# Kernel optimization log

Hardware: AMD Instinct MI355X
Metric: run time of the kernel (lower is better)

## Reference

```python
import jax, jax.numpy as jnp
import numpy as np

EPS = 1e-5
NUM_HEADS = 8
BLOCK_SIZE = 8


def _ln(x, w, b):
    mu = jnp.mean(x, axis=-1, keepdims=True)
    var = jnp.mean((x - mu) ** 2, axis=-1, keepdims=True)
    return (x - mu) * jax.lax.rsqrt(var + EPS) * w + b


def _mha(x, wqkv, bqkv, wo, bo, allowed):
    # x: [b,t,d]; wqkv: [3d,d]; allowed: [t,t] bool (True = attend)
    b, t, d = x.shape
    h, hd = NUM_HEADS, d // NUM_HEADS
    qkv = x @ wqkv.T + bqkv
    q, k, v = jnp.split(qkv, 3, axis=-1)
    q = q.reshape(b, t, h, hd)
    k = k.reshape(b, t, h, hd)
    v = v.reshape(b, t, h, hd)
    scores = jnp.einsum('bihd,bjhd->bhij', q, k) / np.sqrt(hd).astype(x.dtype)
    scores = jnp.where(allowed[None, None], scores, -jnp.inf)
    attn = jax.nn.softmax(scores, axis=-1)
    out = jnp.einsum('bhij,bjhd->bihd', attn, v).reshape(b, t, d)
    return out @ wo.T + bo


def setup_inputs() -> dict:
    key = jax.random.key(0)
    ks = jax.random.split(key, 20)
    B, T, D, FF, L, MAXT = 64, 512, 256, 512, 4, 512
    s = 0.02
    return {
        'latents': jax.random.normal(ks[0], (B, T, D), dtype=jnp.float32),
        'move_ids': jax.random.randint(ks[1], (B, T), 0, 20480),
        'mask': jax.random.randint(ks[2], (B, T), 0, 2).astype(bool),
        'positional': s * jax.random.normal(ks[3], (1, MAXT, D), dtype=jnp.float32),
        'embed_from': s * jax.random.normal(ks[4], (64, D), dtype=jnp.float32),
        'embed_to': s * jax.random.normal(ks[5], (64, D), dtype=jnp.float32),
        'embed_promo': s * jax.random.normal(ks[6], (5, D), dtype=jnp.float32),
        'in_proj_w': s * jax.random.normal(ks[7], (L, 3 * D, D), dtype=jnp.float32),
        'in_proj_b': jnp.zeros((L, 3 * D), dtype=jnp.float32),
        'out_w': s * jax.random.normal(ks[8], (L, D, D), dtype=jnp.float32),
        'out_b': jnp.zeros((L, D), dtype=jnp.float32),
        'fc1_w': s * jax.random.normal(ks[9], (L, FF, D), dtype=jnp.float32),
        'fc1_b': jnp.zeros((L, FF), dtype=jnp.float32),
        'fc2_w': s * jax.random.normal(ks[10], (L, D, FF), dtype=jnp.float32),
        'fc2_b': jnp.zeros((L, D), dtype=jnp.float32),
        'norm_w': jnp.ones((D,), dtype=jnp.float32),
        'norm_b': jnp.zeros((D,), dtype=jnp.float32),
    }


def reference(latents, move_ids, mask, positional, embed_from, embed_to,
              embed_promo, in_proj_w, in_proj_b, out_w, out_b,
              fc1_w, fc1_b, fc2_w, fc2_b, norm_w, norm_b):
    b, t, d = latents.shape
    # move-id decomposition: promo/from/to embedding sum
    promo = move_ids // 4096
    rem = move_ids % 4096
    frm = rem // 64
    to = rem % 64
    x = latents + positional[:, :t, :] + embed_from[frm] + embed_to[to] + embed_promo[promo]
    # block-causal mask: token i may attend j iff block(j) <= block(i)
    bidx = jnp.arange(t) // BLOCK_SIZE
    allowed = bidx[None, :] <= bidx[:, None]
    n_layers = in_proj_w.shape[0]
    for l in range(n_layers):
        # NOTE: the single LayerNorm (norm_w, norm_b) is shared everywhere,
        # exactly as in the original module.
        x = x + _mha(_ln(x, norm_w, norm_b), in_proj_w[l], in_proj_b[l],
                     out_w[l], out_b[l], allowed)
        h1 = jax.nn.relu(_ln(x, norm_w, norm_b) @ fc1_w[l].T + fc1_b[l])
        x = x + h1 @ fc2_w[l].T + fc2_b[l]
    x = _ln(x, norm_w, norm_b)
    return jnp.where(mask[..., None], x, latents)
```

## Files before the change

kernel.cpp:

```cpp
#include <hip/hip_runtime.h>
#include <math.h>

#define Bv  64
#define Tv  512
#define Dv  256
#define FFv 512
#define Lv  4
#define BTv (Bv*Tv)
#define EPSv 1e-5f
#define RS32 0.17677669529663687f

typedef __attribute__((ext_vector_type(8))) short short8;
typedef __attribute__((ext_vector_type(4))) float f32x4;
typedef unsigned short us;

__device__ __forceinline__ us f2bf(float f) {
    union { float f; unsigned u; } v; v.f = f;
    unsigned u = v.u + 0x7FFFu + ((v.u >> 16) & 1u);
    return (us)(u >> 16);
}
__device__ __forceinline__ unsigned pk2(float a, float b) {
    return ((unsigned)f2bf(b) << 16) | (unsigned)f2bf(a);
}
__device__ __forceinline__ float wave_sum(float v) {
#pragma unroll
    for (int o = 32; o > 0; o >>= 1) v += __shfl_xor(v, o);
    return v;
}

__global__ __launch_bounds__(256) void cvtall_kernel(
    const float* __restrict__ qw, const float* __restrict__ ow,
    const float* __restrict__ f1, const float* __restrict__ f2,
    const float* __restrict__ qb,
    us* __restrict__ wq, us* __restrict__ wo, us* __restrict__ w1,
    us* __restrict__ w2, float* __restrict__ sb)
{
    int blk = blockIdx.x, tid = threadIdx.x;
    if (blk < 2048) {
        const float* s; us* d; int i; float sc = 1.0f;
        if (blk < 768)       { i = blk*256 + tid;        s = qw; d = wq;
                               sc = (((i >> 6) % 768) < 256) ? RS32 : 1.0f; }
        else if (blk < 1024) { i = (blk-768)*256 + tid;  s = ow; d = wo; }
        else if (blk < 1536) { i = (blk-1024)*256 + tid; s = f1; d = w1; }
        else                 { i = (blk-1536)*256 + tid; s = f2; d = w2; }
        float4 v = ((const float4*)s)[i];
        ushort4 o;
        o.x = f2bf(v.x*sc); o.y = f2bf(v.y*sc); o.z = f2bf(v.z*sc); o.w = f2bf(v.w*sc);
        ((ushort4*)d)[i] = o;
    } else {
        int i = (blk-2048)*256 + tid;
        sb[i] = qb[i] * (((i % 768) < 256) ? RS32 : 1.0f);
    }
}

__global__ __launch_bounds__(256) void embed_ln_kernel(
    const float* __restrict__ lat, const int* __restrict__ mids,
    const float* __restrict__ pos, const float* __restrict__ ef,
    const float* __restrict__ et,  const float* __restrict__ ep,
    const float* __restrict__ nw,  const float* __restrict__ nb,
    float* __restrict__ x, us* __restrict__ xn)
{
    int bt = blockIdx.x;
    int d  = threadIdx.x;
    int t  = bt & (Tv - 1);
    int id = mids[bt];
    int promo = id >> 12;
    int rem   = id & 4095;
    int frm   = rem >> 6;
    int to    = rem & 63;
    size_t o = (size_t)bt * Dv + d;
    float xv = lat[o] + pos[t*Dv + d] + ef[frm*Dv + d] + et[to*Dv + d] + ep[promo*Dv + d];
    x[o] = xv;
    __shared__ float rs[4], rq[4];
    int wv = d >> 6, lane = d & 63;
    float s  = wave_sum(xv);
    float sq = wave_sum(xv*xv);
    if (lane == 0) { rs[wv] = s; rq[wv] = sq; }
    __syncthreads();
    float mu  = (rs[0]+rs[1]+rs[2]+rs[3]) * (1.0f/Dv);
    float var = (rq[0]+rq[1]+rq[2]+rq[3]) * (1.0f/Dv) - mu*mu;
    float inv = rsqrtf(var + EPSv);
    xn[o] = f2bf((xv - mu)*inv*nw[d] + nb[d]);
}

__global__ __launch_bounds__(256) void final_kernel(
    const float* __restrict__ x, const float* __restrict__ lat,
    const int* __restrict__ mask, const float* __restrict__ w,
    const float* __restrict__ b, float* __restrict__ out)
{
    int wv = threadIdx.x >> 6, lane = threadIdx.x & 63;
    size_t row = (size_t)blockIdx.x * 4 + wv;
    float4 v = ((const float4*)(x + row*Dv))[lane];
    float mu = wave_sum(v.x + v.y + v.z + v.w) * (1.0f/Dv);
    float dx = v.x-mu, dy = v.y-mu, dz = v.z-mu, dw = v.w-mu;
    float var = wave_sum(dx*dx + dy*dy + dz*dz + dw*dw) * (1.0f/Dv);
    float inv = rsqrtf(var + EPSv);
    float4 w4 = ((const float4*)w)[lane];
    float4 b4 = ((const float4*)b)[lane];
    float4 o;
    o.x = dx*inv*w4.x + b4.x;
    o.y = dy*inv*w4.y + b4.y;
    o.z = dz*inv*w4.z + b4.z;
    o.w = dw*inv*w4.w + b4.w;
    if (!mask[row]) o = ((const float4*)(lat + row*Dv))[lane];
    ((float4*)(out + row*Dv))[lane] = o;
}

template<int RELU>
__global__ __launch_bounds__(256) void mm_kernel(
    const us* __restrict__ A, const us* __restrict__ B,
    const float* __restrict__ bias, us* __restrict__ C,
    int M, int N, int K)
{
    __shared__ us As[128*64];
    __shared__ us Bs[128*64];
    int tid  = threadIdx.x;
    int lane = tid & 63;
    int wu   = __builtin_amdgcn_readfirstlane(tid >> 6);
    int m0 = blockIdx.x * 128, n0 = blockIdx.y * 128;
    int wm = wu & 1, wn = wu >> 1;
    f32x4 acc[4][4] = {};
    int srow = lane >> 3;
    int sg   = (lane & 7) ^ srow;
    const us* Ag = A + (size_t)m0 * K + sg*8;
    const us* Bg = B + (size_t)n0 * K + sg*8;
    int cc = lane & 15, q4 = lane >> 4;
    for (int k0 = 0; k0 < K; k0 += 64) {
        __syncthreads();
#pragma unroll
        for (int p = 0; p < 4; p++) {
            int row = wu*32 + p*8;
            __builtin_amdgcn_global_load_lds(
                (const __attribute__((address_space(1))) unsigned int*)(Ag + (size_t)(row + srow)*K + k0),
                (__attribute__((address_space(3))) unsigned int*)(As + row*64),
                16, 0, 0);
            __builtin_amdgcn_global_load_lds(
                (const __attribute__((address_space(1))) unsigned int*)(Bg + (size_t)(row + srow)*K + k0),
                (__attribute__((address_space(3))) unsigned int*)(Bs + row*64),
                16, 0, 0);
        }
        __syncthreads();
#pragma unroll
        for (int h = 0; h < 2; h++) {
            int pg = ((h*4 + q4) ^ (cc & 7)) * 8;
            short8 av[4], bv[4];
#pragma unroll
            for (int i = 0; i < 4; i++)
                av[i] = *(const short8*)(As + (wm*64 + i*16 + cc)*64 + pg);
#pragma unroll
            for (int j = 0; j < 4; j++)
                bv[j] = *(const short8*)(Bs + (wn*64 + j*16 + cc)*64 + pg);
#pragma unroll
            for (int i = 0; i < 4; i++)
#pragma unroll
                for (int j = 0; j < 4; j++)
                    acc[i][j] = __builtin_amdgcn_mfma_f32_16x16x32_bf16(av[i], bv[j], acc[i][j], 0, 0, 0);
        }
    }
#pragma unroll
    for (int j = 0; j < 4; j++) {
        int n = n0 + wn*64 + j*16 + cc;
        float bj = bias[n];
#pragma unroll
        for (int i = 0; i < 4; i++) {
#pragma unroll
            for (int r = 0; r < 4; r++) {
                int m = m0 + wm*64 + i*16 + q4*4 + r;
                float v = acc[i][j][r] + bj;
                if (RELU) v = fmaxf(v, 0.f);
                C[(size_t)m * N + n] = f2bf(v);
            }
        }
    }
}

__global__ __launch_bounds__(256) void mm256_kernel(
    const us* __restrict__ A, const us* __restrict__ B,
    const float* __restrict__ bias, float* __restrict__ x,
    us* __restrict__ xn, const float* __restrict__ nw,
    const float* __restrict__ nb, int M, int K)
{
    __shared__ us As[64*64];
    __shared__ us Bs[256*64];
    __shared__ float red[64][4][2];
    __shared__ float mus[64], rss[64];
    int tid  = threadIdx.x;
    int lane = tid & 63;
    int wu   = __builtin_amdgcn_readfirstlane(tid >> 6);
    int m0 = blockIdx.x * 64;
    f32x4 acc[4][4] = {};
    int srow = lane >> 3;
    int sg   = (lane & 7) ^ srow;
    const us* Ag = A + (size_t)m0 * K + sg*8;
    const us* Bg = B + sg*8;
    int cc = lane & 15, q4 = lane >> 4;
    for (int k0 = 0; k0 < K; k0 += 64) {
        __syncthreads();
#pragma unroll
        for (int p = 0; p < 2; p++) {
            int row = wu*16 + p*8;
            __builtin_amdgcn_global_load_lds(
                (const __attribute__((address_space(1))) unsigned int*)(Ag + (size_t)(row + srow)*K + k0),
                (__attribute__((address_space(3))) unsigned int*)(As + row*64),
                16, 0, 0);
        }
#pragma unroll
        for (int p = 0; p < 8; p++) {
            int row = wu*64 + p*8;
            __builtin_amdgcn_global_load_lds(
                (const __attribute__((address_space(1))) unsigned int*)(Bg + (size_t)(row + srow)*K + k0),
                (__attribute__((address_space(3))) unsigned int*)(Bs + row*64),
                16, 0, 0);
        }
        __syncthreads();
#pragma unroll
        for (int h = 0; h < 2; h++) {
            int pg = ((h*4 + q4) ^ (cc & 7)) * 8;
            short8 av[4], bv[4];
#pragma unroll
            for (int i = 0; i < 4; i++)
                av[i] = *(const short8*)(As + (i*16 + cc)*64 + pg);
#pragma unroll
            for (int j = 0; j < 4; j++)
                bv[j] = *(const short8*)(Bs + (wu*64 + j*16 + cc)*64 + pg);
#pragma unroll
            for (int i = 0; i < 4; i++)
#pragma unroll
                for (int j = 0; j < 4; j++)
                    acc[i][j] = __builtin_amdgcn_mfma_f32_16x16x32_bf16(av[i], bv[j], acc[i][j], 0, 0, 0);
        }
    }
    float bb[4], nwv[4], nbv[4];
#pragma unroll
    for (int j = 0; j < 4; j++) {
        int n = wu*64 + j*16 + cc;
        bb[j] = bias[n]; nwv[j] = nw[n]; nbv[j] = nb[n];
    }
#pragma unroll
    for (int i = 0; i < 4; i++) {
        float s[4] = {0.f,0.f,0.f,0.f}, sq[4] = {0.f,0.f,0.f,0.f};
#pragma unroll
        for (int j = 0; j < 4; j++) {
#pragma unroll
            for (int r = 0; r < 4; r++) {
                int m = m0 + i*16 + q4*4 + r;
                size_t off = (size_t)m * Dv + wu*64 + j*16 + cc;
                float v = acc[i][j][r] + bb[j] + x[off];
                acc[i][j][r] = v;
                x[off] = v;
                s[r] += v; sq[r] += v*v;
            }
        }
#pragma unroll
        for (int r = 0; r < 4; r++) {
#pragma unroll
            for (int o = 1; o < 16; o <<= 1) {
                s[r]  += __shfl_xor(s[r],  o);
                sq[r] += __shfl_xor(sq[r], o);
            }
        }
        if (cc == 0) {
#pragma unroll
            for (int r = 0; r < 4; r++) {
                red[i*16 + q4*4 + r][wu][0] = s[r];
                red[i*16 + q4*4 + r][wu][1] = sq[r];
            }
        }
    }
    __syncthreads();
    if (tid < 64) {
        float ts = red[tid][0][0] + red[tid][1][0] + red[tid][2][0] + red[tid][3][0];
        float tq = red[tid][0][1] + red[tid][1][1] + red[tid][2][1] + red[tid][3][1];
        float mu = ts * (1.0f/Dv);
        float var = tq * (1.0f/Dv) - mu*mu;
        mus[tid] = mu;
        rss[tid] = rsqrtf(var + EPSv);
    }
    __syncthreads();
#pragma unroll
    for (int i = 0; i < 4; i++) {
#pragma unroll
        for (int r = 0; r < 4; r++) {
            int ml = i*16 + q4*4 + r;
            float mu = mus[ml], rv = rss[ml];
#pragma unroll
            for (int j = 0; j < 4; j++) {
                size_t off = (size_t)(m0 + ml) * Dv + wu*64 + j*16 + cc;
                xn[off] = f2bf((acc[i][j][r] - mu)*rv*nwv[j] + nbv[j]);
            }
        }
    }
}

__global__ __launch_bounds__(512) void ffn_kernel(
    const us* __restrict__ W1, const float* __restrict__ b1,
    const us* __restrict__ W2, const float* __restrict__ b2,
    float* __restrict__ x, us* xn,
    const float* __restrict__ nw, const float* __restrict__ nb)
{
    __shared__ us Axn[4*64*64];
    __shared__ us bufB[64*520];
    __shared__ float red[64][2][2];
    __shared__ float mus[64], rss[64];

    int tid  = threadIdx.x;
    int lane = tid & 63;
    int wu   = __builtin_amdgcn_readfirstlane(tid >> 6);
    int m0   = blockIdx.x * 64;
    int srow = lane >> 3;
    int sg   = (lane & 7) ^ srow;
    int cc = lane & 15, q4 = lane >> 4;
    int rw  = (wu & 3) * 16;
    int cw  = (wu >> 2) * 256;
    int cw2 = (wu >> 2) * 128;

#pragma unroll
    for (int j4 = 0; j4 < 4; j4++) {
        int j = wu*4 + j4;
        int kt = j >> 3, p = j & 7;
        __builtin_amdgcn_global_load_lds(
            (const __attribute__((address_space(1))) unsigned int*)(xn + (size_t)(m0 + p*8 + srow)*256 + kt*64 + sg*8),
            (__attribute__((address_space(3))) unsigned int*)(Axn + kt*4096 + p*512),
            16, 0, 0);
    }

    f32x4 acc1[16] = {};
    for (int kt = 0; kt < 4; kt++) {
        __syncthreads();
#pragma unroll
        for (int jj = 0; jj < 8; jj++) {
            int j = wu*8 + jj;
            __builtin_amdgcn_global_load_lds(
                (const __attribute__((address_space(1))) unsigned int*)(W1 + (size_t)(j*8 + srow)*256 + kt*64 + sg*8),
                (__attribute__((address_space(3))) unsigned int*)(bufB + j*512),
                16, 0, 0);
        }
        __syncthreads();
#pragma unroll
        for (int h2 = 0; h2 < 2; h2++) {
            int pg = ((h2*4 + q4) ^ (cc & 7)) * 8;
            short8 af = *(const short8*)(Axn + kt*4096 + (rw + cc)*64 + pg);
#pragma unroll
            for (int jj = 0; jj < 16; jj++) {
                short8 bf = *(const short8*)(bufB + (cw + jj*16 + cc)*64 + pg);
                acc1[jj] = __builtin_amdgcn_mfma_f32_16x16x32_bf16(af, bf, acc1[jj], 0, 0, 0);
            }
        }
    }
    __syncthreads();
#pragma unroll
    for (int jj = 0; jj < 16; jj++) {
        int n = cw + jj*16 + cc;
        float bb = b1[n];
#pragma unroll
        for (int r = 0; r < 4; r++) {
            float v = fmaxf(acc1[jj][r] + bb, 0.f);
            bufB[(rw + q4*4 + r)*520 + n] = f2bf(v);
        }
    }

    f32x4 acc2[8] = {};
    for (int kt2 = 0; kt2 < 8; kt2++) {
        __syncthreads();
#pragma unroll
        for (int j4 = 0; j4 < 4; j4++) {
            int j = wu*4 + j4;
            __builtin_amdgcn_global_load_lds(
                (const __attribute__((address_space(1))) unsigned int*)(W2 + (size_t)(j*8 + srow)*512 + kt2*64 + sg*8),
                (__attribute__((address_space(3))) unsigned int*)(Axn + j*512),
                16, 0, 0);
        }
        __syncthreads();
#pragma unroll
        for (int h2 = 0; h2 < 2; h2++) {
            short8 af = *(const short8*)(bufB + (rw + cc)*520 + kt2*64 + (h2*4 + q4)*8);
            int pg = ((h2*4 + q4) ^ (cc & 7)) * 8;
#pragma unroll
            for (int j2 = 0; j2 < 8; j2++) {
                short8 bf = *(const short8*)(Axn + (cw2 + j2*16 + cc)*64 + pg);
                acc2[j2] = __builtin_amdgcn_mfma_f32_16x16x32_bf16(af, bf, acc2[j2], 0, 0, 0);
            }
        }
    }

    float bb2[8], nwv[8], nbv[8];
#pragma unroll
    for (int j2 = 0; j2 < 8; j2++) {
        int n = cw2 + j2*16 + cc;
        bb2[j2] = b2[n]; nwv[j2] = nw[n]; nbv[j2] = nb[n];
    }
    float s[4] = {0.f,0.f,0.f,0.f}, sq[4] = {0.f,0.f,0.f,0.f};
#pragma unroll
    for (int j2 = 0; j2 < 8; j2++) {
#pragma unroll
        for (int r = 0; r < 4; r++) {
            size_t off = (size_t)(m0 + rw + q4*4 + r) * Dv + cw2 + j2*16 + cc;
            float v = acc2[j2][r] + bb2[j2] + x[off];
            acc2[j2][r] = v;
            x[off] = v;
            s[r] += v; sq[r] += v*v;
        }
    }
#pragma unroll
    for (int r = 0; r < 4; r++) {
#pragma unroll
        for (int o = 1; o < 16; o <<= 1) {
            s[r]  += __shfl_xor(s[r],  o);
            sq[r] += __shfl_xor(sq[r], o);
        }
    }
    if (cc == 0) {
#pragma unroll
        for (int r = 0; r < 4; r++) {
            red[rw + q4*4 + r][wu >> 2][0] = s[r];
            red[rw + q4*4 + r][wu >> 2][1] = sq[r];
        }
    }
    __syncthreads();
    if (tid < 64) {
        float ts = red[tid][0][0] + red[tid][1][0];
        float tq = red[tid][0][1] + red[tid][1][1];
        float mu = ts * (1.0f/Dv);
        float var = tq * (1.0f/Dv) - mu*mu;
        mus[tid] = mu;
        rss[tid] = rsqrtf(var + EPSv);
    }
    __syncthreads();
#pragma unroll
    for (int r = 0; r < 4; r++) {
        int ml = rw + q4*4 + r;
        float mu = mus[ml], rv = rss[ml];
#pragma unroll
        for (int j2 = 0; j2 < 8; j2++) {
            size_t off = (size_t)(m0 + ml) * Dv + cw2 + j2*16 + cc;
            xn[off] = f2bf((acc2[j2][r] - mu)*rv*nwv[j2] + nbv[j2]);
        }
    }
}

__global__ __launch_bounds__(256) void attn_kernel(
    const us* __restrict__ qkv, us* __restrict__ ao)
{
    int blk = blockIdx.x;
    int b  = blk & 63;
    int h  = (blk >> 6) & 7;
    int qt = blk >> 9;
    int i0 = qt << 6;
    int tid = threadIdx.x;
    int lane = tid & 63;
    int wu = tid >> 6;

    __shared__ us Ks[2][64][40];
    __shared__ us Vt[2][32][72];
    __shared__ us Ps[4][16][72];
    __shared__ float Ls[4][16];

    size_t rowbase = (size_t)b * Tv;
    int c = lane & 15, q4 = lane >> 4;

    short8 qfrag = *(const short8*)(qkv + (rowbase + i0 + wu*16 + c)*768 + h*32 + q4*8);

    int skey = tid >> 2, sdc = (tid & 3) << 3;
    int vkey = tid & 63, vg = tid >> 6;
    const us* kgp = qkv + (rowbase + skey)*768 + 256 + h*32 + sdc;
    const us* vgp = qkv + (rowbase + vkey)*768 + 512 + h*32 + vg*8;

    f32x4 oacc[2] = {};
    float lsum = 0.f;
    int ntiles = qt + 1;

    short8 kreg = *(const short8*)(kgp);
    short8 vreg = *(const short8*)(vgp);
    *(short8*)&Ks[0][skey][sdc] = kreg;
#pragma unroll
    for (int j = 0; j < 8; j++) Vt[0][vg*8 + j][vkey] = vreg[j];
    if (ntiles > 1) {
        kreg = *(const short8*)(kgp + 64*768);
        vreg = *(const short8*)(vgp + 64*768);
    }
    __syncthreads();

    for (int kt = 0; kt < ntiles; kt++) {
        int cur = kt & 1;
        if (kt + 1 < ntiles) {
            *(short8*)&Ks[cur^1][skey][sdc] = kreg;
#pragma unroll
            for (int j = 0; j < 8; j++) Vt[cur^1][vg*8 + j][vkey] = vreg[j];
        }
        if (kt + 2 < ntiles) {
            kreg = *(const short8*)(kgp + (size_t)(kt+2)*64*768);
            vreg = *(const short8*)(vgp + (size_t)(kt+2)*64*768);
        }

        f32x4 st[4];
#pragma unroll
        for (int jt = 0; jt < 4; jt++) {
            short8 kf = *(const short8*)&Ks[cur][jt*16 + c][q4*8];
            st[jt] = __builtin_amdgcn_mfma_f32_16x16x32_bf16(kf, qfrag, (f32x4){0.f,0.f,0.f,0.f}, 0, 0, 0);
        }
        bool diag = (kt == ntiles - 1);
#pragma unroll
        for (int jt = 0; jt < 4; jt++) {
            float msk = (!diag || (2*jt + (q4 >> 1) <= 2*wu + (c >> 3))) ? 1.f : 0.f;
            float p0 = __expf(st[jt][0]) * msk;
            float p1 = __expf(st[jt][1]) * msk;
            float p2 = __expf(st[jt][2]) * msk;
            float p3 = __expf(st[jt][3]) * msk;
            lsum += p0 + p1 + p2 + p3;
            uint2 w2; w2.x = pk2(p0, p1); w2.y = pk2(p2, p3);
            *(uint2*)&Ps[wu][c][jt*16 + q4*4] = w2;
        }
#pragma unroll
        for (int kk = 0; kk < 2; kk++) {
            short8 pf = *(const short8*)&Ps[wu][c][kk*32 + q4*8];
#pragma unroll
            for (int dt = 0; dt < 2; dt++) {
                short8 vf = *(const short8*)&Vt[cur][dt*16 + c][kk*32 + q4*8];
                oacc[dt] = __builtin_amdgcn_mfma_f32_16x16x32_bf16(pf, vf, oacc[dt], 0, 0, 0);
            }
        }
        __syncthreads();
    }

    float l = lsum;
    l += __shfl_xor(l, 16);
    l += __shfl_xor(l, 32);
    if (q4 == 0) Ls[wu][c] = 1.0f / l;
    float4 lv4 = *(const float4*)&Ls[wu][q4*4];
#pragma unroll
    for (int dt = 0; dt < 2; dt++) {
#pragma unroll
        for (int r = 0; r < 4; r++) {
            float li = (r == 0) ? lv4.x : (r == 1) ? lv4.y : (r == 2) ? lv4.z : lv4.w;
            ao[(rowbase + i0 + wu*16 + q4*4 + r)*256 + h*32 + dt*16 + c] = f2bf(oacc[dt][r] * li);
        }
    }
}

extern "C" void kernel_launch(void* const* d_in, const int* in_sizes, int n_in,
                              void* d_out, int out_size, void* d_ws, size_t ws_size,
                              hipStream_t stream)
{
    const float* latents    = (const float*)d_in[0];
    const int*   move_ids   = (const int*)  d_in[1];
    const int*   mask       = (const int*)  d_in[2];
    const float* positional = (const float*)d_in[3];
    const float* embed_from = (const float*)d_in[4];
    const float* embed_to   = (const float*)d_in[5];
    const float* embed_promo= (const float*)d_in[6];
    const float* in_proj_w  = (const float*)d_in[7];
    const float* in_proj_b  = (const float*)d_in[8];
    const float* out_w      = (const float*)d_in[9];
    const float* out_b      = (const float*)d_in[10];
    const float* fc1_w      = (const float*)d_in[11];
    const float* fc1_b      = (const float*)d_in[12];
    const float* fc2_w      = (const float*)d_in[13];
    const float* fc2_b      = (const float*)d_in[14];
    const float* norm_w     = (const float*)d_in[15];
    const float* norm_b     = (const float*)d_in[16];
    float* out = (float*)d_out;

    float* x   = (float*)d_ws;
    float* sb  = x + (size_t)BTv * Dv;
    us* xn  = (us*)(sb + Lv*768);
    us* qkv = xn + (size_t)BTv * Dv;
    us* ao  = qkv + (size_t)BTv * 768;
    us* h1  = ao + (size_t)BTv * Dv;
    us* wq  = h1 + (size_t)BTv * FFv;
    us* wo  = wq + (size_t)Lv * 768 * Dv;
    us* w1  = wo + (size_t)Lv * Dv * Dv;
    us* w2  = w1 + (size_t)Lv * FFv * Dv;

    cvtall_kernel<<<2060, 256, 0, stream>>>(in_proj_w, out_w, fc1_w, fc2_w,
                                            in_proj_b, wq, wo, w1, w2, sb);

    embed_ln_kernel<<<BTv, 256, 0, stream>>>(latents, move_ids, positional,
        embed_from, embed_to, embed_promo, norm_w, norm_b, x, xn);

    for (int l = 0; l < Lv; l++) {
        mm_kernel<0><<<dim3(BTv/128, 768/128), 256, 0, stream>>>(
            xn, wq + (size_t)l*768*Dv, sb + l*768, qkv, BTv, 768, Dv);
        attn_kernel<<<Bv*8*(Tv/64), 256, 0, stream>>>(qkv, ao);
        mm256_kernel<<<BTv/64, 256, 0, stream>>>(
            ao, wo + (size_t)l*Dv*Dv, out_b + l*Dv, x, xn, norm_w, norm_b,
            BTv, Dv);
        ffn_kernel<<<BTv/64, 512, 0, stream>>>(
            w1 + (size_t)l*FFv*Dv, fc1_b + l*FFv,
            w2 + (size_t)l*Dv*FFv, fc2_b + l*Dv,
            x, xn, norm_w, norm_b);
    }
    final_kernel<<<BTv/4, 256, 0, stream>>>(x, latents, mask, norm_w, norm_b, out);
}
```

Measured before the change: 652.1 us.

## Load FFN weights directly from global into registers instead of staging in LDS

The FFN kernel stops staging activation and weight tiles through LDS with global_load_lds and barriers. Each wave now loads its A fragments and W1/W2 fragments straight from global memory into registers, and keeps only the hidden activation tile in LDS. It also adds a min-blocks-per-CU hint to launch bounds to raise occupancy. This removes most barriers and LDS traffic, but gives up cooperative reuse, so each wave issues many more global loads (partly served from cache) and register pressure rises.

```diff
diff --git a/kernel.cpp b/kernel.cpp
--- a/kernel.cpp
+++ b/kernel.cpp
@@ -292,14 +292,13 @@
     }
 }
 
-__global__ __launch_bounds__(512) void ffn_kernel(
+__global__ __launch_bounds__(512, 4) void ffn_kernel(
     const us* __restrict__ W1, const float* __restrict__ b1,
     const us* __restrict__ W2, const float* __restrict__ b2,
     float* __restrict__ x, us* xn,
     const float* __restrict__ nw, const float* __restrict__ nb)
 {
-    __shared__ us Axn[4*64*64];
-    __shared__ us bufB[64*520];
+    __shared__ us h1s[64*520];
     __shared__ float red[64][2][2];
     __shared__ float mus[64], rss[64];
 
@@ -307,78 +306,54 @@
     int lane = tid & 63;
     int wu   = __builtin_amdgcn_readfirstlane(tid >> 6);
     int m0   = blockIdx.x * 64;
-    int srow = lane >> 3;
-    int sg   = (lane & 7) ^ srow;
     int cc = lane & 15, q4 = lane >> 4;
     int rw  = (wu & 3) * 16;
     int cw  = (wu >> 2) * 256;
     int cw2 = (wu >> 2) * 128;
 
-#pragma unroll
-    for (int j4 = 0; j4 < 4; j4++) {
-        int j = wu*4 + j4;
-        int kt = j >> 3, p = j & 7;
-        __builtin_amdgcn_global_load_lds(
-            (const __attribute__((address_space(1))) unsigned int*)(xn + (size_t)(m0 + p*8 + srow)*256 + kt*64 + sg*8),
-            (__attribute__((address_space(3))) unsigned int*)(Axn + kt*4096 + p*512),
-            16, 0, 0);
-    }
-
-    f32x4 acc1[16] = {};
-    for (int kt = 0; kt < 4; kt++) {
-        __syncthreads();
-#pragma unroll
-        for (int jj = 0; jj < 8; jj++) {
-            int j = wu*8 + jj;
-            __builtin_amdgcn_global_load_lds(
-                (const __attribute__((address_space(1))) unsigned int*)(W1 + (size_t)(j*8 + srow)*256 + kt*64 + sg*8),
-                (__attribute__((address_space(3))) unsigned int*)(bufB + j*512),
-                16, 0, 0);
-        }
-        __syncthreads();
-#pragma unroll
-        for (int h2 = 0; h2 < 2; h2++) {
-            int pg = ((h2*4 + q4) ^ (cc & 7)) * 8;
-            short8 af = *(const short8*)(Axn + kt*4096 + (rw + cc)*64 + pg);
-#pragma unroll
-            for (int jj = 0; jj < 16; jj++) {
-                short8 bf = *(const short8*)(bufB + (cw + jj*16 + cc)*64 + pg);
-                acc1[jj] = __builtin_amdgcn_mfma_f32_16x16x32_bf16(af, bf, acc1[jj], 0, 0, 0);
-            }
-        }
-    }
-    __syncthreads();
-#pragma unroll
-    for (int jj = 0; jj < 16; jj++) {
-        int n = cw + jj*16 + cc;
-        float bb = b1[n];
-#pragma unroll
-        for (int r = 0; r < 4; r++) {
-            float v = fmaxf(acc1[jj][r] + bb, 0.f);
-            bufB[(rw + q4*4 + r)*520 + n] = f2bf(v);
-        }
-    }
+    short8 av[8];
+    {
+        const us* xrow = xn + (size_t)(m0 + rw + cc) * 256 + q4*8;
+#pragma unroll
+        for (int t = 0; t < 8; t++)
+            av[t] = *(const short8*)(xrow + t*32);
+    }
+    {
+        const us* w1p = W1 + (size_t)(cw + cc) * 256 + q4*8;
+#pragma unroll 4
+        for (int jj = 0; jj < 16; jj++) {
+            f32x4 acc = {0.f, 0.f, 0.f, 0.f};
+#pragma unroll
+            for (int t = 0; t < 8; t++) {
+                short8 bf = *(const short8*)(w1p + (size_t)jj*16*256 + t*32);
+                acc = __builtin_amdgcn_mfma_f32_16x16x32_bf16(av[t], bf, acc, 0, 0, 0);
+            }
+            int n = cw + jj*16 + cc;
+            float bb = b1[n];
+#pragma unroll
+            for (int r = 0; r < 4; r++) {
+                float v = fmaxf(acc[r] + bb, 0.f);
+                h1s[(rw + q4*4 + r)*520 + n] = f2bf(v);
+            }
+        }
+    }
+    __syncthreads();
 
     f32x4 acc2[8] = {};
-    for (int kt2 = 0; kt2 < 8; kt2++) {
-        __syncthreads();
-#pragma unroll
-        for (int j4 = 0; j4 < 4; j4++) {
-            int j = wu*4 + j4;
-            __builtin_amdgcn_global_load_lds(
-                (const __attribute__((address_space(1))) unsigned int*)(W2 + (size_t)(j*8 + srow)*512 + kt2*64 + sg*8),
-                (__attribute__((address_space(3))) unsigned int*)(Axn + j*512),
-                16, 0, 0);
-        }
-        __syncthreads();
-#pragma unroll
-        for (int h2 = 0; h2 < 2; h2++) {
-            short8 af = *(const short8*)(bufB + (rw + cc)*520 + kt2*64 + (h2*4 + q4)*8);
-            int pg = ((h2*4 + q4) ^ (cc & 7)) * 8;
-#pragma unroll
+    {
+        const us* w2p = W2 + (size_t)(cw2 + cc) * 512 + q4*8;
+#pragma unroll
+        for (int kh = 0; kh < 2; kh++) {
+            short8 af[8];
+#pragma unroll
+            for (int t = 0; t < 8; t++)
+                af[t] = *(const short8*)(h1s + (rw + cc)*520 + kh*256 + t*32 + q4*8);
             for (int j2 = 0; j2 < 8; j2++) {
-                short8 bf = *(const short8*)(Axn + (cw2 + j2*16 + cc)*64 + pg);
-                acc2[j2] = __builtin_amdgcn_mfma_f32_16x16x32_bf16(af, bf, acc2[j2], 0, 0, 0);
+#pragma unroll
+                for (int t = 0; t < 8; t++) {
+                    short8 bf = *(const short8*)(w2p + (size_t)j2*16*512 + kh*256 + t*32);
+                    acc2[j2] = __builtin_amdgcn_mfma_f32_16x16x32_bf16(af[t], bf, acc2[j2], 0, 0, 0);
+                }
             }
         }
     }
```

Result: slower. 980.8 us (+50.4%).
